# Kernel optimization log

Hardware: AMD Instinct MI355X
Metric: run time of the kernel (lower is better)

## Reference

```python
import jax, jax.numpy as jnp
import numpy as np

B, SEQ, OBS, HID = 32, 50, 1024, 256


def setup_inputs() -> dict:
    key = jax.random.key(0)
    k = jax.random.split(key, 6)
    y = jax.random.normal(k[0], (B, SEQ, OBS), jnp.float32)
    logdet = jax.random.normal(k[1], (B * SEQ,), jnp.float32)
    U_param = jax.random.normal(k[2], (HID, HID), jnp.float32)
    V_param = jax.random.normal(k[3], (HID, HID), jnp.float32)
    # torch init sets alpha to small constant 0.001; use small positive values
    alpha = jax.random.uniform(k[4], (HID,), jnp.float32) * 0.01
    # C initialized as orthonormal-ish (svd-projected xavier); scale to unit-norm columns
    C = jax.random.normal(k[5], (OBS, HID), jnp.float32) / np.sqrt(OBS).astype(np.float32)
    return {"y": y, "logdet": logdet, "U_param": U_param, "V_param": V_param,
            "alpha": alpha, "C": C}


def _unitary(Up):
    """Product of dim Householder reflections, combined by pairwise doubling."""
    dim = Up.shape[0]
    Un = Up / jnp.linalg.norm(Up, axis=1, keepdims=True)
    # UH[i] = I - 2 u_i u_i^T   -> (dim, dim, dim)
    M = jnp.eye(dim, dtype=Up.dtype)[None] - 2.0 * Un[:, :, None] * Un[:, None, :]
    n = dim
    while n > 1:  # log2(dim) fixed steps (multi_matmul_power_of_two)
        n //= 2
        M = jnp.matmul(M[:n], M[n:])
    return M[0]


def reference(y, logdet, U_param, V_param, alpha, C):
    U = _unitary(U_param)
    V = _unitary(V_param)
    S = 1.0 - jnp.clip(jnp.abs(alpha), 0.0, 1.0)          # SV()
    A = U @ (S[None, :] * V.T)                             # build_A

    s = y.shape[1]
    obs, hid = C.shape

    # build_O_A: O = [C; C A; C A^2; ...] via scan (matrix-power recurrence)
    def step(T, _):
        return T @ A, T
    _, Os = jax.lax.scan(step, C, None, length=s)          # (s, obs, hid)
    O = Os.reshape(s * obs, hid)

    Y = y.reshape(y.shape[0], -1)                          # (b, s*obs)

    # torch.gels(Y.t(), O): least-squares solve, x0 detached
    x0 = jax.lax.stop_gradient(
        jnp.linalg.lstsq(jax.lax.stop_gradient(O), jax.lax.stop_gradient(Y.T))[0]
    )                                                      # (hid, b)

    Yhat = O @ x0                                          # (s*obs, b)
    w = Y.T - Yhat
    M = jnp.float32(obs)                                   # prod(xflat.shape[1:])
    loss = 0.5 * jnp.mean(w ** 2) + jnp.mean((logdet / M) ** 2)
    return loss


if __name__ == "__main__":
    print(reference(**setup_inputs()))
```

## Files before the change

kernel.cpp:

```cpp
#include <hip/hip_runtime.h>

#define HID 256
#define OBS 1024
#define SEQ 50
#define BATCH 32
#define SO (SEQ*OBS)

struct DevWS {
  float ub[2][HID][HID];
  float C2[2][HID][HID];
  float ZT[2][HID][HID];
  float U[HID][HID];
  float V[HID][HID];
  float A[HID][HID];
  float A2[HID][HID];
  float A4[HID][HID];
  float A8[HID][HID];
  float A16[HID][HID];
  float A32[HID][HID];
  float Cg[HID][HID];
  float G2[HID][HID];
  float Grun[HID][HID];
  float T[HID][HID];
  float T2[HID][HID];
  float G18[HID][HID];
  float G32b[HID][HID];
  float Gfin[HID][HID];
  float Zt[SEQ][HID*BATCH];
  float Rb[2][25][HID*BATCH];
  float psum[1025];
  float s1b[32];
};
__device__ DevWS g;

__device__ __forceinline__ float* sel(int c){
  switch(c){
    case 0:  return &g.ub[0][0][0];
    case 1:  return &g.ub[1][0][0];
    case 4:  return &g.C2[0][0][0];
    case 5:  return &g.C2[1][0][0];
    case 6:  return &g.ZT[0][0][0];
    case 7:  return &g.ZT[1][0][0];
    case 8:  return &g.U[0][0];
    case 9:  return &g.V[0][0];
    case 10: return &g.A[0][0];
    case 11: return &g.A2[0][0];
    case 12: return &g.A4[0][0];
    case 13: return &g.A8[0][0];
    case 14: return &g.A16[0][0];
    case 15: return &g.A32[0][0];
    case 16: return &g.Cg[0][0];
    case 17: return &g.G2[0][0];
    case 18: return &g.Grun[0][0];
    case 19: return &g.T[0][0];
    case 20: return &g.T2[0][0];
    case 21: return &g.G18[0][0];
    case 22: return &g.G32b[0][0];
    case 23: return &g.Gfin[0][0];
    case 24: return &g.Zt[0][0];
    case 25: return &g.Rb[0][0][0];
    default: return &g.Rb[1][0][0];
  }
}

__device__ __forceinline__ int bitrev8(int x){
  x = ((x & 0x55) << 1) | ((x >> 1) & 0x55);
  x = ((x & 0x33) << 2) | ((x >> 2) & 0x33);
  x = ((x & 0x0F) << 4) | ((x >> 4) & 0x0F);
  return x;
}

__global__ __launch_bounds__(256) void k_prep(const float* __restrict__ y,
                                              const float* __restrict__ logdet,
                                              const float* __restrict__ Up,
                                              const float* __restrict__ Vp,
                                              const float* __restrict__ Cm){
  __shared__ float As[16][36];
  __shared__ float Bs[16][36];
  __shared__ float red[256];
  const int bx = blockIdx.x;
  const int t = threadIdx.x;
  if(bx < 512){
    int mat = bx >> 8, j = bx & 255;
    int src = bitrev8(j);
    const float* P = mat ? Vp : Up;
    float x = P[src*HID + t];
    red[t] = x*x; __syncthreads();
    for(int s=128; s>0; s>>=1){ if(t<s) red[t]+=red[t+s]; __syncthreads(); }
    g.ub[mat][j][t] = x * rsqrtf(red[0]);
    return;
  }
  if(bx < 1536){
    int bi = bx - 512;
    const float4* y4 = reinterpret_cast<const float4*>(y);
    const int n4 = (BATCH*SO)/4;
    float s = 0.f;
    for(int i = bi*256 + t; i < n4; i += 1024*256){
      float4 v = y4[i];
      s += v.x*v.x + v.y*v.y + v.z*v.z + v.w*v.w;
    }
    red[t] = s; __syncthreads();
    for(int st=128; st>0; st>>=1){ if(t<st) red[t]+=red[t+st]; __syncthreads(); }
    if(t==0) g.psum[bi] = red[0];
    return;
  }
  if(bx == 1536){
    float s = 0.f;
    for(int i = t; i < BATCH*SEQ; i += 256){ float v = logdet[i]; s += v*v; }
    red[t] = s; __syncthreads();
    for(int st=128; st>0; st>>=1){ if(t<st) red[t]+=red[t+st]; __syncthreads(); }
    if(t==0) g.psum[1024] = red[0];
    return;
  }
  {
    int tile = bx - 1537;
    int tx = t & 15, ty = t >> 4;
    int m0 = (tile>>3)*32, n0 = (tile&7)*32;
    float acc[2][2] = {{0.f,0.f},{0.f,0.f}};
    for(int o0=0; o0<OBS; o0+=16){
      int r = t>>4, cp = (t&15)*2;
      float2 a = *reinterpret_cast<const float2*>(&Cm[(o0+r)*HID + m0 + cp]);
      As[r][cp] = a.x; As[r][cp+1] = a.y;
      float2 b = *reinterpret_cast<const float2*>(&Cm[(o0+r)*HID + n0 + cp]);
      Bs[r][cp] = b.x; Bs[r][cp+1] = b.y;
      __syncthreads();
      #pragma unroll
      for(int kk=0; kk<16; kk++){
        float a0 = As[kk][ty*2], a1 = As[kk][ty*2+1];
        float b0 = Bs[kk][tx*2], b1 = Bs[kk][tx*2+1];
        acc[0][0]+=a0*b0; acc[0][1]+=a0*b1; acc[1][0]+=a1*b0; acc[1][1]+=a1*b1;
      }
      __syncthreads();
    }
    #pragma unroll
    for(int i2=0;i2<2;i2++)
    #pragma unroll
    for(int j2=0;j2<2;j2++)
      g.Cg[m0+ty*2+i2][n0+tx*2+j2] = acc[i2][j2];
  }
}

__global__ __launch_bounds__(1024) void k_CtY(const float* __restrict__ y,
                                              const float* __restrict__ C){
  const int tt = blockIdx.x;
  __shared__ float ys[256][36];
  const int h = threadIdx.x >> 2, bq = threadIdx.x & 3;
  float acc[8] = {0,0,0,0,0,0,0,0};
  for(int ot=0; ot<4; ot++){
    for(int e=threadIdx.x; e<32*256; e+=1024){
      int b = e>>8, o = e&255;
      ys[o][b] = y[b*SO + tt*OBS + ot*256 + o];
    }
    __syncthreads();
    for(int o=0; o<256; o++){
      float cv = C[(ot*256+o)*HID + h];
      float4 v0 = *reinterpret_cast<const float4*>(&ys[o][bq*8]);
      float4 v1 = *reinterpret_cast<const float4*>(&ys[o][bq*8+4]);
      acc[0]+=cv*v0.x; acc[1]+=cv*v0.y; acc[2]+=cv*v0.z; acc[3]+=cv*v0.w;
      acc[4]+=cv*v1.x; acc[5]+=cv*v1.y; acc[6]+=cv*v1.z; acc[7]+=cv*v1.w;
    }
    __syncthreads();
  }
  #pragma unroll
  for(int j=0;j<8;j++) g.Zt[tt][h*32 + bq*8 + j] = acc[j];
}

__global__ __launch_bounds__(1024) void k_wy(){
  const int m = blockIdx.x;
  const int t = threadIdx.x;
  __shared__ float c2s[32][256];
  __shared__ float ws[32][256];
  for(int p=0; p<8; p++){
    const int k0 = p*32;
    for(int e=t; e<32*256; e+=1024){
      int k = e>>8, i = e&255;
      c2s[k][i] = (i < k0+k) ? g.C2[m][k0+k][i] : 0.f;
    }
    __syncthreads();
    {
      int d = t & 255, kg = t>>8;
      float acc[8] = {0,0,0,0,0,0,0,0};
      for(int i=0; i<k0; i++){
        float zv = g.ZT[m][i][d];
        #pragma unroll
        for(int kk=0; kk<8; kk++) acc[kk] += zv * c2s[kg*8+kk][i];
      }
      #pragma unroll
      for(int kk=0; kk<8; kk++) ws[kg*8+kk][d] = acc[kk];
    }
    __syncthreads();
    if(t < 256){
      const int d = t;
      float zreg[32];
      #pragma unroll
      for(int j=0;j<32;j++) zreg[j] = 0.f;
      #pragma unroll
      for(int k=0; k<32; k++){
        float a0=0.f,a1=0.f,a2=0.f,a3=0.f;
        #pragma unroll
        for(int j=0;j<32;j+=4){
          a0 += zreg[j]  *c2s[k][k0+j];
          a1 += zreg[j+1]*c2s[k][k0+j+1];
          a2 += zreg[j+2]*c2s[k][k0+j+2];
          a3 += zreg[j+3]*c2s[k][k0+j+3];
        }
        float acc = (a0+a1)+(a2+a3);
        zreg[k] = 2.f*(g.ub[m][k0+k][d] - ws[k][d] - acc);
      }
      #pragma unroll
      for(int k=0; k<32; k++) g.ZT[m][k0+k][d] = zreg[k];
    }
    __syncthreads();
  }
}

#define F_TRANSA   1
#define F_NEGID    2
#define F_ACC      4
#define F_TRANSB   8
#define F_SCALECOL 16
#define F_RLEVEL   32

struct GD { int cA, cB, cC, cD, flags, npair; };
struct GArgs { GD d[3]; int pre[3]; int nd; };

__global__ __launch_bounds__(256) void k_gemmN(GArgs ga, const float* __restrict__ alpha){
  int blk = blockIdx.x;
  int di = 0;
  if(ga.nd > 1 && blk >= ga.pre[1]) di = 1;
  if(ga.nd > 2 && blk >= ga.pre[2]) di = 2;
  const GD d = ga.d[di];
  const int local = blk - ga.pre[di];
  const int t = threadIdx.x;
  __shared__ float As[16][36];
  __shared__ float Bs[16][36];
  const int tx = t & 15, ty = t >> 4;

  if(d.flags & F_RLEVEL){
    const float* P  = sel(d.cA);
    const float* In = sel(d.cB);
    float* Out = sel(d.cC);
    const int j = local >> 3, mt = local & 7;
    if(j >= d.npair){
      const float* src = In + (size_t)(2*j)*(HID*BATCH) + mt*1024;
      float* dst = Out + (size_t)j*(HID*BATCH) + mt*1024;
      *reinterpret_cast<float4*>(dst + t*4) = *reinterpret_cast<const float4*>(src + t*4);
      return;
    }
    const float* B1 = In + (size_t)(2*j+1)*(HID*BATCH);
    const float* D0 = In + (size_t)(2*j)*(HID*BATCH);
    float* C0 = Out + (size_t)j*(HID*BATCH);
    const int m0 = mt*32;
    float acc[2][2] = {{0.f,0.f},{0.f,0.f}};
    for(int k0=0; k0<HID; k0+=16){
      { int kk=t>>4, mm=(t&15)*2;
        float2 a = *reinterpret_cast<const float2*>(&P[(k0+kk)*HID + m0+mm]);
        As[kk][mm]=a.x; As[kk][mm+1]=a.y; }
      { int rb=t>>4, cb=(t&15)*2;
        float2 b = *reinterpret_cast<const float2*>(&B1[(k0+rb)*BATCH + cb]);
        Bs[rb][cb]=b.x; Bs[rb][cb+1]=b.y; }
      __syncthreads();
      #pragma unroll
      for(int kk=0; kk<16; kk++){
        float a0=As[kk][ty*2], a1=As[kk][ty*2+1];
        float b0=Bs[kk][tx*2], b1=Bs[kk][tx*2+1];
        acc[0][0]+=a0*b0; acc[0][1]+=a0*b1; acc[1][0]+=a1*b0; acc[1][1]+=a1*b1;
      }
      __syncthreads();
    }
    #pragma unroll
    for(int i2=0;i2<2;i2++)
    #pragma unroll
    for(int j2=0;j2<2;j2++){
      int r=m0+ty*2+i2, c=tx*2+j2;
      C0[r*BATCH+c] = D0[r*BATCH+c] + acc[i2][j2];
    }
    return;
  }

  const float* A = sel(d.cA);
  const float* B = sel(d.cB);
  float* Cp = sel(d.cC);
  const float* Dp = sel(d.cD);
  const int m0 = (local>>3)*32, n0 = (local&7)*32;
  float acc[2][2] = {{0.f,0.f},{0.f,0.f}};
  for(int k0=0; k0<HID; k0+=16){
    if(d.flags & F_TRANSA){
      int kk=t>>4, mm=(t&15)*2;
      float2 a = *reinterpret_cast<const float2*>(&A[(k0+kk)*HID + m0+mm]);
      As[kk][mm]=a.x; As[kk][mm+1]=a.y;
    } else {
      int r=t>>3, c=(t&7)*2;
      float2 a = *reinterpret_cast<const float2*>(&A[(m0+r)*HID + k0+c]);
      As[c][r]=a.x; As[c+1][r]=a.y;
    }
    if(d.flags & F_TRANSB){
      int cb=t>>3, rb=(t&7)*2;
      float2 v = *reinterpret_cast<const float2*>(&B[(n0+cb)*HID + k0+rb]);
      Bs[rb][cb]=v.x; Bs[rb+1][cb]=v.y;
    } else {
      int rb=t>>4, cb=(t&15)*2;
      float2 b = *reinterpret_cast<const float2*>(&B[(k0+rb)*HID + n0+cb]);
      Bs[rb][cb]=b.x; Bs[rb][cb+1]=b.y;
    }
    __syncthreads();
    #pragma unroll
    for(int kk=0; kk<16; kk++){
      float a0=As[kk][ty*2], a1=As[kk][ty*2+1];
      float b0=Bs[kk][tx*2], b1=Bs[kk][tx*2+1];
      acc[0][0]+=a0*b0; acc[0][1]+=a0*b1; acc[1][0]+=a1*b0; acc[1][1]+=a1*b1;
    }
    __syncthreads();
  }
  float sc0=1.f, sc1=1.f;
  if(d.flags & F_SCALECOL){
    sc0 = 1.0f - fminf(fabsf(alpha[n0+tx*2]),   1.0f);
    sc1 = 1.0f - fminf(fabsf(alpha[n0+tx*2+1]), 1.0f);
  }
  #pragma unroll
  for(int i2=0;i2<2;i2++)
  #pragma unroll
  for(int j2=0;j2<2;j2++){
    int r=m0+ty*2+i2, c=n0+tx*2+j2;
    float v = acc[i2][j2];
    if(d.flags & F_ACC) v += Dp[r*HID+c];
    if(d.flags & F_SCALECOL) v *= (j2 ? sc1 : sc0);
    if(d.flags & F_NEGID) v = (r==c ? 1.0f : 0.0f) - v;
    Cp[r*HID+c] = v;
  }
}

#define CG_ITERS 10
__global__ __launch_bounds__(1024) void k_cg(){
  const int tid = threadIdx.x;
  const int i = tid & 255;
  const int q = tid >> 8;
  const int lane = tid & 63;
  const int wv = tid >> 6;
  const int b0 = blockIdx.x * 4;
  __shared__ float p_s[256][4];
  __shared__ float partf[4][256][4];
  __shared__ float red1[16];
  __shared__ float s_rz[4], s_pap[4], s_rzn[4], s_be[4], s_s1[4];

  float gr[64];
  const float* Gf = &g.Gfin[0][0];
  #pragma unroll
  for(int j=0;j<64;j++) gr[j] = Gf[(64*q+j)*HID + i];
  const float dinv = 1.0f / Gf[i*(HID+1)];

  float rcur = g.Rb[1][0][i*BATCH + b0 + q];
  p_s[i][q] = rcur*dinv;
  if(tid<4) s_s1[tid]=0.f;
  __syncthreads();

  {
    float v = dinv*rcur*rcur;
    v+=__shfl_down(v,32);v+=__shfl_down(v,16);v+=__shfl_down(v,8);
    v+=__shfl_down(v,4);v+=__shfl_down(v,2);v+=__shfl_down(v,1);
    if(lane==0) red1[wv]=v;
    __syncthreads();
    if(tid<4) s_rz[tid]=red1[tid*4]+red1[tid*4+1]+red1[tid*4+2]+red1[tid*4+3];
    __syncthreads();
  }

  for(int it=0; it<CG_ITERS; it++){
    float pa0=0.f,pa1=0.f,pa2=0.f,pa3=0.f;
    #pragma unroll
    for(int j=0;j<64;j++){
      const float4 pv = *reinterpret_cast<const float4*>(&p_s[64*q+j][0]);
      const float gv = gr[j];
      pa0 = fmaf(gv,pv.x,pa0); pa1 = fmaf(gv,pv.y,pa1);
      pa2 = fmaf(gv,pv.z,pa2); pa3 = fmaf(gv,pv.w,pa3);
    }
    float4 w4; w4.x=pa0; w4.y=pa1; w4.z=pa2; w4.w=pa3;
    *reinterpret_cast<float4*>(&partf[q][i][0]) = w4;
    __syncthreads();
    const float ap = partf[0][i][q]+partf[1][i][q]+partf[2][i][q]+partf[3][i][q];
    const float pvl = p_s[i][q];
    {
      float v = pvl*ap;
      v+=__shfl_down(v,32);v+=__shfl_down(v,16);v+=__shfl_down(v,8);
      v+=__shfl_down(v,4);v+=__shfl_down(v,2);v+=__shfl_down(v,1);
      if(lane==0) red1[wv]=v;
      __syncthreads();
      if(tid<4) s_pap[tid]=red1[tid*4]+red1[tid*4+1]+red1[tid*4+2]+red1[tid*4+3];
      __syncthreads();
    }
    const float al = s_rz[q]/fmaxf(s_pap[q],1e-30f);
    rcur = rcur - al*ap;
    {
      float v = dinv*rcur*rcur;
      v+=__shfl_down(v,32);v+=__shfl_down(v,16);v+=__shfl_down(v,8);
      v+=__shfl_down(v,4);v+=__shfl_down(v,2);v+=__shfl_down(v,1);
      if(lane==0) red1[wv]=v;
      __syncthreads();
      if(tid<4) s_rzn[tid]=red1[tid*4]+red1[tid*4+1]+red1[tid*4+2]+red1[tid*4+3];
      __syncthreads();
    }
    if(tid<4){
      const float alb = s_rz[tid]/fmaxf(s_pap[tid],1e-30f);
      s_s1[tid] += alb*s_rz[tid];
      s_be[tid]  = s_rzn[tid]/fmaxf(s_rz[tid],1e-30f);
      s_rz[tid]  = s_rzn[tid];
    }
    __syncthreads();
    p_s[i][q] = dinv*rcur + s_be[q]*p_s[i][q];
    __syncthreads();
  }
  if(tid<4) g.s1b[b0+tid] = s_s1[tid];
}

__global__ __launch_bounds__(256) void k_fin(float* __restrict__ out){
  const int t = threadIdx.x;
  __shared__ float red[4];
  float s = g.psum[t] + g.psum[t+256] + g.psum[t+512] + g.psum[t+768];
  s += __shfl_down(s,32); s += __shfl_down(s,16); s += __shfl_down(s,8);
  s += __shfl_down(s,4);  s += __shfl_down(s,2);  s += __shfl_down(s,1);
  if((t&63)==0) red[t>>6]=s;
  __syncthreads();
  if(t==0){
    float sy2 = red[0]+red[1]+red[2]+red[3];
    float t1 = 0.f;
    for(int b=0;b<32;b++) t1 += g.s1b[b];
    float sld = g.psum[1024];
    float mw = (sy2 - t1) / (float)(SO*BATCH);
    out[0] = 0.5f*mw + sld / ((float)(BATCH*SEQ) * (float)OBS * (float)OBS);
  }
}

struct LB { GArgs ga; int total; };
static inline GD sq(int cA,int cB,int cC,int cD,int flags){ GD d; d.cA=cA;d.cB=cB;d.cC=cC;d.cD=cD;d.flags=flags;d.npair=0; return d; }
static inline GD rl(int cP,int cin,int cout,int npair){ GD d; d.cA=cP;d.cB=cin;d.cC=cout;d.cD=0;d.flags=F_RLEVEL;d.npair=npair; return d; }
static inline LB mk1(GD a,int ba){ LB l; l.ga.d[0]=a; l.ga.pre[0]=0; l.ga.pre[1]=ba; l.ga.pre[2]=ba; l.ga.nd=1; l.total=ba; return l; }
static inline LB mk2(GD a,int ba,GD b,int bb){ LB l; l.ga.d[0]=a; l.ga.d[1]=b; l.ga.pre[0]=0; l.ga.pre[1]=ba; l.ga.pre[2]=ba+bb; l.ga.nd=2; l.total=ba+bb; return l; }
static inline LB mk3(GD a,int ba,GD b,int bb,GD c,int bc){ LB l; l.ga.d[0]=a; l.ga.d[1]=b; l.ga.d[2]=c; l.ga.pre[0]=0; l.ga.pre[1]=ba; l.ga.pre[2]=ba+bb; l.ga.nd=3; l.total=ba+bb+bc; return l; }

extern "C" void kernel_launch(void* const* d_in, const int* in_sizes, int n_in,
                              void* d_out, int out_size, void* d_ws, size_t ws_size,
                              hipStream_t stream){
  const float* y      = (const float*)d_in[0];
  const float* logdet = (const float*)d_in[1];
  const float* Up     = (const float*)d_in[2];
  const float* Vp     = (const float*)d_in[3];
  const float* alpha  = (const float*)d_in[4];
  const float* Cm     = (const float*)d_in[5];
  float* out = (float*)d_out;

  k_prep<<<dim3(1601), dim3(256), 0, stream>>>(y, logdet, Up, Vp, Cm);
  k_CtY<<<dim3(SEQ), dim3(1024), 0, stream>>>(y, Cm);
  { LB l = mk2(sq(0,0,4,4,F_TRANSB),64, sq(1,1,5,5,F_TRANSB),64);
    k_gemmN<<<l.total,256,0,stream>>>(l.ga, alpha); }
  k_wy<<<dim3(2), dim3(1024), 0, stream>>>();
  { LB l = mk2(sq(6,0,8,8,F_TRANSA|F_NEGID),64, sq(7,1,9,9,F_TRANSA|F_NEGID),64);
    k_gemmN<<<l.total,256,0,stream>>>(l.ga, alpha); }
  { LB l = mk1(sq(8,9,10,10,F_TRANSB|F_SCALECOL),64);
    k_gemmN<<<l.total,256,0,stream>>>(l.ga, alpha); }
  { LB l = mk2(sq(10,10,11,0,0),64, sq(10,16,19,0,F_TRANSA),64);
    k_gemmN<<<l.total,256,0,stream>>>(l.ga, alpha); }
  { LB l = mk2(sq(19,10,17,16,F_ACC),64, rl(10,24,25,25),200);
    k_gemmN<<<l.total,256,0,stream>>>(l.ga, alpha); }
  { LB l = mk2(sq(11,11,12,0,0),64, sq(11,17,19,0,F_TRANSA),64);
    k_gemmN<<<l.total,256,0,stream>>>(l.ga, alpha); }
  { LB l = mk2(sq(19,11,18,17,F_ACC),64, rl(11,25,26,12),104);
    k_gemmN<<<l.total,256,0,stream>>>(l.ga, alpha); }
  { LB l = mk2(sq(12,12,13,0,0),64, sq(12,18,19,0,F_TRANSA),64);
    k_gemmN<<<l.total,256,0,stream>>>(l.ga, alpha); }
  { LB l = mk2(sq(19,12,18,18,F_ACC),64, rl(12,26,25,6),56);
    k_gemmN<<<l.total,256,0,stream>>>(l.ga, alpha); }
  { LB l = mk2(sq(13,13,14,0,0),64, sq(13,18,19,0,F_TRANSA),64);
    k_gemmN<<<l.total,256,0,stream>>>(l.ga, alpha); }
  { LB l = mk2(sq(19,13,18,18,F_ACC),64, rl(13,25,26,3),32);
    k_gemmN<<<l.total,256,0,stream>>>(l.ga, alpha); }
  { LB l = mk3(sq(14,14,15,0,0),64, sq(14,18,19,0,F_TRANSA),64, sq(14,17,20,0,F_TRANSA),64);
    k_gemmN<<<l.total,256,0,stream>>>(l.ga, alpha); }
  { LB l = mk3(sq(19,14,22,18,F_ACC),64, sq(20,14,21,18,F_ACC),64, rl(14,26,25,2),16);
    k_gemmN<<<l.total,256,0,stream>>>(l.ga, alpha); }
  { LB l = mk2(sq(15,21,19,0,F_TRANSA),64, rl(15,25,26,1),8);
    k_gemmN<<<l.total,256,0,stream>>>(l.ga, alpha); }
  { LB l = mk1(sq(19,15,23,22,F_ACC),64);
    k_gemmN<<<l.total,256,0,stream>>>(l.ga, alpha); }

  k_cg<<<dim3(8), dim3(1024), 0, stream>>>();
  k_fin<<<dim3(1), dim3(256), 0, stream>>>(out);
}
```

Measured before the change: 562.5 us.

## Fuse paired Gram GEMMs into one launch and restructure WY kernel accumulation

Adds a fused GEMM mode that computes X^T G X in a single block: each block recomputes a full 256x32 column strip of G·X in shared memory, then multiplies by X^T. This roughly halves the launch count in the doubling chain. The cost is redundant work, since each of the 8 row blocks per column strip recomputes that strip, and shared memory grows to about 52KB, which lowers occupancy. The WY kernel is also rewritten to keep running W accumulators in registers spread across thread groups and to stage C2 and ub in shared memory. This replaces the per-panel reload of ZT from global memory.

```diff
diff --git a/kernel.cpp b/kernel.cpp
--- a/kernel.cpp
+++ b/kernel.cpp
@@ -168,47 +168,73 @@
 __global__ __launch_bounds__(1024) void k_wy(){
   const int m = blockIdx.x;
   const int t = threadIdx.x;
-  __shared__ float c2s[32][256];
+  const int d = t & 255;
+  const int q = t >> 8;
+  __shared__ float c2ft[256][32];
+  __shared__ float zsd[256][36];
+  __shared__ float ubs[32][256];
   __shared__ float ws[32][256];
-  for(int p=0; p<8; p++){
+  float wacc[64];
+  #pragma unroll
+  for(int j=0;j<64;j++) wacc[j]=0.f;
+  const float* C2m = &g.C2[m][0][0];
+  const float* ubm = &g.ub[m][0][0];
+
+  for(int p=0;p<8;p++){
     const int k0 = p*32;
-    for(int e=t; e<32*256; e+=1024){
-      int k = e>>8, i = e&255;
-      c2s[k][i] = (i < k0+k) ? g.C2[m][k0+k][i] : 0.f;
-    }
-    __syncthreads();
-    {
-      int d = t & 255, kg = t>>8;
-      float acc[8] = {0,0,0,0,0,0,0,0};
-      for(int i=0; i<k0; i++){
-        float zv = g.ZT[m][i][d];
+    for(int e=t;e<8192;e+=1024){
+      int k=e>>5, i=e&31;
+      c2ft[k][i] = C2m[k*HID + k0 + i];
+    }
+    for(int e=t;e<8192;e+=1024){
+      int kl=e>>8, dd=e&255;
+      ubs[kl][dd] = ubm[(k0+kl)*HID + dd];
+    }
+    if(q == (p>>1)){
+      if(p & 1){
         #pragma unroll
-        for(int kk=0; kk<8; kk++) acc[kk] += zv * c2s[kg*8+kk][i];
-      }
+        for(int kl=0;kl<32;kl++) ws[kl][d] = wacc[32+kl];
+      } else {
+        #pragma unroll
+        for(int kl=0;kl<32;kl++) ws[kl][d] = wacc[kl];
+      }
+    }
+    __syncthreads();
+    if(t < 256){
       #pragma unroll
-      for(int kk=0; kk<8; kk++) ws[kg*8+kk][d] = acc[kk];
-    }
-    __syncthreads();
-    if(t < 256){
-      const int d = t;
-      float zreg[32];
+      for(int k=0;k<32;k++){
+        float acc = 0.f;
+        #pragma unroll
+        for(int j0=0;j0+4<=k;j0+=4){
+          float4 cz = *reinterpret_cast<const float4*>(&c2ft[k0+k][j0]);
+          float4 zz = *reinterpret_cast<const float4*>(&zsd[d][j0]);
+          acc += cz.x*zz.x + cz.y*zz.y + cz.z*zz.z + cz.w*zz.w;
+        }
+        #pragma unroll
+        for(int j=(k&~3);j<k;j++) acc += c2ft[k0+k][j]*zsd[d][j];
+        float z = 2.f*(ubs[k][d] - ws[k][d] - acc);
+        zsd[d][k] = z;
+        g.ZT[m][k0+k][d] = z;
+      }
+    }
+    __syncthreads();
+    if(p < 7){
+      const int kfirst = k0 + 32;
       #pragma unroll
-      for(int j=0;j<32;j++) zreg[j] = 0.f;
-      #pragma unroll
-      for(int k=0; k<32; k++){
-        float a0=0.f,a1=0.f,a2=0.f,a3=0.f;
+      for(int i0=0;i0<32;i0+=8){
+        float4 za = *reinterpret_cast<const float4*>(&zsd[d][i0]);
+        float4 zb = *reinterpret_cast<const float4*>(&zsd[d][i0+4]);
         #pragma unroll
-        for(int j=0;j<32;j+=4){
-          a0 += zreg[j]  *c2s[k][k0+j];
-          a1 += zreg[j+1]*c2s[k][k0+j+1];
-          a2 += zreg[j+2]*c2s[k][k0+j+2];
-          a3 += zreg[j+3]*c2s[k][k0+j+3];
+        for(int j=0;j<64;j++){
+          int k = q*64 + j;
+          if(k >= kfirst){
+            float4 ca = *reinterpret_cast<const float4*>(&c2ft[k][i0]);
+            float4 cb = *reinterpret_cast<const float4*>(&c2ft[k][i0+4]);
+            wacc[j] += ca.x*za.x+ca.y*za.y+ca.z*za.z+ca.w*za.w
+                     + cb.x*zb.x+cb.y*zb.y+cb.z*zb.z+cb.w*zb.w;
+          }
         }
-        float acc = (a0+a1)+(a2+a3);
-        zreg[k] = 2.f*(g.ub[m][k0+k][d] - ws[k][d] - acc);
-      }
-      #pragma unroll
-      for(int k=0; k<32; k++) g.ZT[m][k0+k][d] = zreg[k];
+      }
     }
     __syncthreads();
   }
@@ -220,21 +246,79 @@
 #define F_TRANSB   8
 #define F_SCALECOL 16
 #define F_RLEVEL   32
+#define F_GDBL     64
 
 struct GD { int cA, cB, cC, cD, flags, npair; };
-struct GArgs { GD d[3]; int pre[3]; int nd; };
+struct GArgs { GD d[4]; int pre[4]; int nd; };
 
 __global__ __launch_bounds__(256) void k_gemmN(GArgs ga, const float* __restrict__ alpha){
   int blk = blockIdx.x;
   int di = 0;
-  if(ga.nd > 1 && blk >= ga.pre[1]) di = 1;
-  if(ga.nd > 2 && blk >= ga.pre[2]) di = 2;
+  #pragma unroll
+  for(int s=1;s<4;s++) if(ga.nd > s && blk >= ga.pre[s]) di = s;
   const GD d = ga.d[di];
   const int local = blk - ga.pre[di];
   const int t = threadIdx.x;
-  __shared__ float As[16][36];
-  __shared__ float Bs[16][36];
   const int tx = t & 15, ty = t >> 4;
+  __shared__ float sm[13408];
+  #define AS(a,b) sm[(a)*36+(b)]
+  #define BS(a,b) sm[576+(a)*36+(b)]
+
+  if(d.flags & F_GDBL){
+    const float* X  = sel(d.cA);
+    const float* Gm = sel(d.cB);
+    float* Outp = sel(d.cC);
+    const float* E  = sel(d.cD);
+    float* Ws = sm;
+    float* Gs = sm + 8704;
+    float* Xb = sm + 12832;
+    const int m0=(local>>3)*32, n0=(local&7)*32;
+    float accW[8][4];
+    #pragma unroll
+    for(int r=0;r<8;r++){ accW[r][0]=0.f;accW[r][1]=0.f;accW[r][2]=0.f;accW[r][3]=0.f; }
+    for(int k0=0;k0<HID;k0+=16){
+      for(int e=t;e<4096;e+=256){ int kk=e>>8, r=e&255; Gs[kk*258+r] = Gm[(k0+kk)*HID + r]; }
+      for(int e=t;e<512;e+=256){ int kk=e>>5, c=e&31; Xb[kk*36+c] = X[(k0+kk)*HID + n0 + c]; }
+      __syncthreads();
+      #pragma unroll
+      for(int kk=0;kk<16;kk++){
+        float b0 = Xb[kk*36+tx*2], b1 = Xb[kk*36+tx*2+1];
+        #pragma unroll
+        for(int r0=0;r0<8;r0++){
+          float a0 = Gs[kk*258 + r0*32 + ty*2];
+          float a1 = Gs[kk*258 + r0*32 + ty*2 + 1];
+          accW[r0][0]+=a0*b0; accW[r0][1]+=a0*b1; accW[r0][2]+=a1*b0; accW[r0][3]+=a1*b1;
+        }
+      }
+      __syncthreads();
+    }
+    #pragma unroll
+    for(int r0=0;r0<8;r0++){
+      Ws[(r0*32+ty*2)*34 + tx*2]     = accW[r0][0];
+      Ws[(r0*32+ty*2)*34 + tx*2+1]   = accW[r0][1];
+      Ws[(r0*32+ty*2+1)*34 + tx*2]   = accW[r0][2];
+      Ws[(r0*32+ty*2+1)*34 + tx*2+1] = accW[r0][3];
+    }
+    __syncthreads();
+    float acc2[4]={0.f,0.f,0.f,0.f};
+    for(int k0=0;k0<HID;k0+=16){
+      for(int e=t;e<512;e+=256){ int kk=e>>5, mm=e&31; Xb[kk*36+mm] = X[(k0+kk)*HID + m0 + mm]; }
+      __syncthreads();
+      #pragma unroll
+      for(int kk=0;kk<16;kk++){
+        float a0 = Xb[kk*36+ty*2], a1 = Xb[kk*36+ty*2+1];
+        float b0 = Ws[(k0+kk)*34 + tx*2], b1 = Ws[(k0+kk)*34 + tx*2+1];
+        acc2[0]+=a0*b0; acc2[1]+=a0*b1; acc2[2]+=a1*b0; acc2[3]+=a1*b1;
+      }
+      __syncthreads();
+    }
+    const int r=m0+ty*2, c=n0+tx*2;
+    Outp[r*HID+c]       = E[r*HID+c]       + acc2[0];
+    Outp[r*HID+c+1]     = E[r*HID+c+1]     + acc2[1];
+    Outp[(r+1)*HID+c]   = E[(r+1)*HID+c]   + acc2[2];
+    Outp[(r+1)*HID+c+1] = E[(r+1)*HID+c+1] + acc2[3];
+    return;
+  }
 
   if(d.flags & F_RLEVEL){
     const float* P  = sel(d.cA);
@@ -255,15 +339,15 @@
     for(int k0=0; k0<HID; k0+=16){
       { int kk=t>>4, mm=(t&15)*2;
         float2 a = *reinterpret_cast<const float2*>(&P[(k0+kk)*HID + m0+mm]);
-        As[kk][mm]=a.x; As[kk][mm+1]=a.y; }
+        AS(kk,mm)=a.x; AS(kk,mm+1)=a.y; }
       { int rb=t>>4, cb=(t&15)*2;
         float2 b = *reinterpret_cast<const float2*>(&B1[(k0+rb)*BATCH + cb]);
-        Bs[rb][cb]=b.x; Bs[rb][cb+1]=b.y; }
+        BS(rb,cb)=b.x; BS(rb,cb+1)=b.y; }
       __syncthreads();
       #pragma unroll
       for(int kk=0; kk<16; kk++){
-        float a0=As[kk][ty*2], a1=As[kk][ty*2+1];
-        float b0=Bs[kk][tx*2], b1=Bs[kk][tx*2+1];
+        float a0=AS(kk,ty*2), a1=AS(kk,ty*2+1);
+        float b0=BS(kk,tx*2), b1=BS(kk,tx*2+1);
         acc[0][0]+=a0*b0; acc[0][1]+=a0*b1; acc[1][0]+=a1*b0; acc[1][1]+=a1*b1;
       }
       __syncthreads();
@@ -288,26 +372,26 @@
     if(d.flags & F_TRANSA){
       int kk=t>>4, mm=(t&15)*2;
       float2 a = *reinterpret_cast<const float2*>(&A[(k0+kk)*HID + m0+mm]);
-      As[kk][mm]=a.x; As[kk][mm+1]=a.y;
+      AS(kk,mm)=a.x; AS(kk,mm+1)=a.y;
     } else {
       int r=t>>3, c=(t&7)*2;
       float2 a = *reinterpret_cast<const float2*>(&A[(m0+r)*HID + k0+c]);
-      As[c][r]=a.x; As[c+1][r]=a.y;
+      AS(c,r)=a.x; AS(c+1,r)=a.y;
     }
     if(d.flags & F_TRANSB){
       int cb=t>>3, rb=(t&7)*2;
       float2 v = *reinterpret_cast<const float2*>(&B[(n0+cb)*HID + k0+rb]);
-      Bs[rb][cb]=v.x; Bs[rb+1][cb]=v.y;
+      BS(rb,cb)=v.x; BS(rb+1,cb)=v.y;
     } else {
       int rb=t>>4, cb=(t&15)*2;
       float2 b = *reinterpret_cast<const float2*>(&B[(k0+rb)*HID + n0+cb]);
-      Bs[rb][cb]=b.x; Bs[rb][cb+1]=b.y;
+      BS(rb,cb)=b.x; BS(rb,cb+1)=b.y;
     }
     __syncthreads();
     #pragma unroll
     for(int kk=0; kk<16; kk++){
-      float a0=As[kk][ty*2], a1=As[kk][ty*2+1];
-      float b0=Bs[kk][tx*2], b1=Bs[kk][tx*2+1];
+      float a0=AS(kk,ty*2), a1=AS(kk,ty*2+1);
+      float b0=BS(kk,tx*2), b1=BS(kk,tx*2+1);
       acc[0][0]+=a0*b0; acc[0][1]+=a0*b1; acc[1][0]+=a1*b0; acc[1][1]+=a1*b1;
     }
     __syncthreads();
@@ -328,6 +412,8 @@
     if(d.flags & F_NEGID) v = (r==c ? 1.0f : 0.0f) - v;
     Cp[r*HID+c] = v;
   }
+  #undef AS
+  #undef BS
 }
 
 #define CG_ITERS 10
@@ -431,10 +517,14 @@
 
 struct LB { GArgs ga; int total; };
 static inline GD sq(int cA,int cB,int cC,int cD,int flags){ GD d; d.cA=cA;d.cB=cB;d.cC=cC;d.cD=cD;d.flags=flags;d.npair=0; return d; }
+static inline GD gdb(int cX,int cG,int cOut,int cE){ GD d; d.cA=cX;d.cB=cG;d.cC=cOut;d.cD=cE;d.flags=F_GDBL;d.npair=0; return d; }
 static inline GD rl(int cP,int cin,int cout,int npair){ GD d; d.cA=cP;d.cB=cin;d.cC=cout;d.cD=0;d.flags=F_RLEVEL;d.npair=npair; return d; }
-static inline LB mk1(GD a,int ba){ LB l; l.ga.d[0]=a; l.ga.pre[0]=0; l.ga.pre[1]=ba; l.ga.pre[2]=ba; l.ga.nd=1; l.total=ba; return l; }
-static inline LB mk2(GD a,int ba,GD b,int bb){ LB l; l.ga.d[0]=a; l.ga.d[1]=b; l.ga.pre[0]=0; l.ga.pre[1]=ba; l.ga.pre[2]=ba+bb; l.ga.nd=2; l.total=ba+bb; return l; }
-static inline LB mk3(GD a,int ba,GD b,int bb,GD c,int bc){ LB l; l.ga.d[0]=a; l.ga.d[1]=b; l.ga.d[2]=c; l.ga.pre[0]=0; l.ga.pre[1]=ba; l.ga.pre[2]=ba+bb; l.ga.nd=3; l.total=ba+bb+bc; return l; }
+static inline LB mkN(const GD* ds, const int* bs, int n){
+  LB l; int acc=0;
+  for(int i=0;i<4;i++){ l.ga.pre[i]=0; }
+  for(int i=0;i<n;i++){ l.ga.d[i]=ds[i]; l.ga.pre[i]=acc; acc+=bs[i]; }
+  l.ga.nd=n; l.total=acc; return l;
+}
 
 extern "C" void kernel_launch(void* const* d_in, const int* in_sizes, int n_in,
                               void* d_out, int out_size, void* d_ws, size_t ws_size,
@@ -449,37 +539,25 @@
 
   k_prep<<<dim3(1601), dim3(256), 0, stream>>>(y, logdet, Up, Vp, Cm);
   k_CtY<<<dim3(SEQ), dim3(1024), 0, stream>>>(y, Cm);
-  { LB l = mk2(sq(0,0,4,4,F_TRANSB),64, sq(1,1,5,5,F_TRANSB),64);
-    k_gemmN<<<l.total,256,0,stream>>>(l.ga, alpha); }
+  { GD ds[2]={sq(0,0,4,4,F_TRANSB), sq(1,1,5,5,F_TRANSB)}; int bs[2]={64,64};
+    LB l=mkN(ds,bs,2); k_gemmN<<<l.total,256,0,stream>>>(l.ga, alpha); }
   k_wy<<<dim3(2), dim3(1024), 0, stream>>>();
-  { LB l = mk2(sq(6,0,8,8,F_TRANSA|F_NEGID),64, sq(7,1,9,9,F_TRANSA|F_NEGID),64);
-    k_gemmN<<<l.total,256,0,stream>>>(l.ga, alpha); }
-  { LB l = mk1(sq(8,9,10,10,F_TRANSB|F_SCALECOL),64);
-    k_gemmN<<<l.total,256,0,stream>>>(l.ga, alpha); }
-  { LB l = mk2(sq(10,10,11,0,0),64, sq(10,16,19,0,F_TRANSA),64);
-    k_gemmN<<<l.total,256,0,stream>>>(l.ga, alpha); }
-  { LB l = mk2(sq(19,10,17,16,F_ACC),64, rl(10,24,25,25),200);
-    k_gemmN<<<l.total,256,0,stream>>>(l.ga, alpha); }
-  { LB l = mk2(sq(11,11,12,0,0),64, sq(11,17,19,0,F_TRANSA),64);
-    k_gemmN<<<l.total,256,0,stream>>>(l.ga, alpha); }
-  { LB l = mk2(sq(19,11,18,17,F_ACC),64, rl(11,25,26,12),104);
-    k_gemmN<<<l.total,256,0,stream>>>(l.ga, alpha); }
-  { LB l = mk2(sq(12,12,13,0,0),64, sq(12,18,19,0,F_TRANSA),64);
-    k_gemmN<<<l.total,256,0,stream>>>(l.ga, alpha); }
-  { LB l = mk2(sq(19,12,18,18,F_ACC),64, rl(12,26,25,6),56);
-    k_gemmN<<<l.total,256,0,stream>>>(l.ga, alpha); }
-  { LB l = mk2(sq(13,13,14,0,0),64, sq(13,18,19,0,F_TRANSA),64);
-    k_gemmN<<<l.total,256,0,stream>>>(l.ga, alpha); }
-  { LB l = mk2(sq(19,13,18,18,F_ACC),64, rl(13,25,26,3),32);
-    k_gemmN<<<l.total,256,0,stream>>>(l.ga, alpha); }
-  { LB l = mk3(sq(14,14,15,0,0),64, sq(14,18,19,0,F_TRANSA),64, sq(14,17,20,0,F_TRANSA),64);
-    k_gemmN<<<l.total,256,0,stream>>>(l.ga, alpha); }
-  { LB l = mk3(sq(19,14,22,18,F_ACC),64, sq(20,14,21,18,F_ACC),64, rl(14,26,25,2),16);
-    k_gemmN<<<l.total,256,0,stream>>>(l.ga, alpha); }
-  { LB l = mk2(sq(15,21,19,0,F_TRANSA),64, rl(15,25,26,1),8);
-    k_gemmN<<<l.total,256,0,stream>>>(l.ga, alpha); }
-  { LB l = mk1(sq(19,15,23,22,F_ACC),64);
-    k_gemmN<<<l.total,256,0,stream>>>(l.ga, alpha); }
+  { GD ds[2]={sq(6,0,8,8,F_TRANSA|F_NEGID), sq(7,1,9,9,F_TRANSA|F_NEGID)}; int bs[2]={64,64};
+    LB l=mkN(ds,bs,2); k_gemmN<<<l.total,256,0,stream>>>(l.ga, alpha); }
+  { GD ds[1]={sq(8,9,10,10,F_TRANSB|F_SCALECOL)}; int bs[1]={64};
+    LB l=mkN(ds,bs,1); k_gemmN<<<l.total,256,0,stream>>>(l.ga, alpha); }
+  { GD ds[3]={sq(10,10,11,0,0), gdb(10,16,17,16), rl(10,24,25,25)}; int bs[3]={64,64,200};
+    LB l=mkN(ds,bs,3); k_gemmN<<<l.total,256,0,stream>>>(l.ga, alpha); }
+  { GD ds[3]={sq(11,11,12,0,0), gdb(11,17,18,17), rl(11,25,26,12)}; int bs[3]={64,64,104};
+    LB l=mkN(ds,bs,3); k_gemmN<<<l.total,256,0,stream>>>(l.ga, alpha); }
+  { GD ds[3]={sq(12,12,13,0,0), gdb(12,18,19,18), rl(12,26,25,6)}; int bs[3]={64,64,56};
+    LB l=mkN(ds,bs,3); k_gemmN<<<l.total,256,0,stream>>>(l.ga, alpha); }
+  { GD ds[3]={sq(13,13,14,0,0), gdb(13,19,18,19), rl(13,25,26,3)}; int bs[3]={64,64,32};
+    LB l=mkN(ds,bs,3); k_gemmN<<<l.total,256,0,stream>>>(l.ga, alpha); }
+  { GD ds[4]={sq(14,14,15,0,0), gdb(14,18,22,18), gdb(14,17,21,18), rl(14,26,25,2)}; int bs[4]={64,64,64,16};
+    LB l=mkN(ds,bs,4); k_gemmN<<<l.total,256,0,stream>>>(l.ga, alpha); }
+  { GD ds[2]={gdb(15,21,23,22), rl(15,25,26,1)}; int bs[2]={64,8};
+    LB l=mkN(ds,bs,2); k_gemmN<<<l.total,256,0,stream>>>(l.ga, alpha); }
 
   k_cg<<<dim3(8), dim3(1024), 0, stream>>>();
   k_fin<<<dim3(1), dim3(256), 0, stream>>>(out);
```

Measured after the change: 761.5 us. 35.4% more time.
